# Optimization experiments

Hardware: AMD Instinct MI355X
Metric: run time of the kernel (lower is better)

## Reference

```python
import jax, jax.numpy as jnp
import numpy as np

B, C, H, W = 4, 96, 56, 56
K0, K1, DIL, HID = 5, 7, 3, 4  # HID: ConvMlp(dim, expansion, drop) => hidden_features = int(mlp_ratio) = 4 (repo quirk)
EPS = 1e-5


def _conv(x, w, b, pad, dil=1, groups=1):
    y = jax.lax.conv_general_dilated(x, w, (1, 1), [(pad, pad), (pad, pad)],
                                     rhs_dilation=(dil, dil),
                                     dimension_numbers=('NCHW', 'OIHW', 'NCHW'),
                                     feature_group_count=groups)
    return y + b[None, :, None, None]


def _conv1x1(x, w, b):
    return jnp.einsum('bchw,oc->bohw', x, w) + b[None, :, None, None]


def _ln(x, g, b):
    # LayerNormProxy: LayerNorm over channel dim of NCHW
    mu = jnp.mean(x, axis=1, keepdims=True)
    v = jnp.var(x, axis=1, keepdims=True)
    return (x - mu) * jax.lax.rsqrt(v + EPS) * g[None, :, None, None] + b[None, :, None, None]


def _gelu(x):
    return jax.nn.gelu(x, approximate=False)  # torch nn.GELU default = exact erf


def _deform_dw(x, ow, ob, dw, db, k, dil, pad):
    # DeformConv2d wrapper: offsets from a same-geometry conv, then depthwise deformable conv.
    Bx, Cx, Hx, Wx = x.shape
    P = k * k
    off = _conv(x, ow, ob, pad, dil).reshape(Bx, P, 2, Hx, Wx)  # [B,P,(y,x),H,W]
    ky = (jnp.repeat(jnp.arange(k), k) * dil - pad).astype(x.dtype)  # row-major kernel grid
    kx = (jnp.tile(jnp.arange(k), k) * dil - pad).astype(x.dtype)
    py = jnp.arange(Hx, dtype=x.dtype)[None, None, :, None] + ky[None, :, None, None] + off[:, :, 0]
    px = jnp.arange(Wx, dtype=x.dtype)[None, None, None, :] + kx[None, :, None, None] + off[:, :, 1]
    y0 = jnp.floor(py)
    x0 = jnp.floor(px)
    wy = py - y0
    wx = px - x0
    xf = x.reshape(Bx, Cx, Hx * Wx)

    def corner(yi, xi):
        valid = (yi >= 0) & (yi < Hx) & (xi >= 0) & (xi < Wx)
        idx = (jnp.clip(yi, 0, Hx - 1).astype(jnp.int32) * Wx
               + jnp.clip(xi, 0, Wx - 1).astype(jnp.int32)).reshape(Bx, -1)
        g = jax.vmap(lambda a, i: jnp.take(a, i, axis=1))(xf, idx).reshape(Bx, Cx, P, Hx, Wx)
        return g * valid[:, None].astype(x.dtype)

    v = (corner(y0, x0) * ((1 - wy) * (1 - wx))[:, None]
         + corner(y0, x0 + 1) * ((1 - wy) * wx)[:, None]
         + corner(y0 + 1, x0) * (wy * (1 - wx))[:, None]
         + corner(y0 + 1, x0 + 1) * (wy * wx)[:, None])  # [B,C,P,H,W]
    return jnp.einsum('bcphw,cp->bchw', v, dw) + db[None, :, None, None]


def setup_inputs() -> dict:
    key = jax.random.key(0)
    ks = iter(jax.random.split(key, 32))

    def rn(shape, s=1.0):
        return jax.random.normal(next(ks), shape, jnp.float32) * s

    f32 = jnp.float32
    return {
        'x': rn((B, C, H, W)),
        'g1n': jnp.ones((C,), f32), 'b1n': jnp.zeros((C,), f32),
        'p1w': rn((C, C), 1 / np.sqrt(C)), 'p1b': jnp.zeros((C,), f32),
        'o0w': rn((2 * K0 * K0, C, K0, K0), 0.05 / np.sqrt(C * K0 * K0)), 'o0b': jnp.zeros((2 * K0 * K0,), f32),
        'd0w': rn((C, K0 * K0), 1 / np.sqrt(K0 * K0)), 'd0b': jnp.zeros((C,), f32),
        'o1w': rn((2 * K1 * K1, C, K1, K1), 0.05 / np.sqrt(C * K1 * K1)), 'o1b': jnp.zeros((2 * K1 * K1,), f32),
        'd1w': rn((C, K1 * K1), 1 / np.sqrt(K1 * K1)), 'd1b': jnp.zeros((C,), f32),
        'c1w': rn((C, C), 1 / np.sqrt(C)), 'c1b': jnp.zeros((C,), f32),
        'p2w': rn((C, C), 1 / np.sqrt(C)), 'p2b': jnp.zeros((C,), f32),
        'ls1': jnp.full((C,), 0.01, f32),
        'g2n': jnp.ones((C,), f32), 'b2n': jnp.zeros((C,), f32),
        'f1w': rn((HID, C), 1 / np.sqrt(C)), 'f1b': jnp.zeros((HID,), f32),
        'dww': rn((HID, 1, 3, 3), 1 / 3.0), 'dwb': jnp.zeros((HID,), f32),
        'f2w': rn((C, HID), 1 / np.sqrt(HID)), 'f2b': jnp.zeros((C,), f32),
        'ls2': jnp.full((C,), 0.01, f32),
    }


def reference(x, g1n, b1n, p1w, p1b, o0w, o0b, d0w, d0b, o1w, o1b, d1w, d1b,
              c1w, c1b, p2w, p2b, ls1, g2n, b2n, f1w, f1b, dww, dwb, f2w, f2b, ls2):
    # attention branch
    y = _ln(x, g1n, b1n)
    shortcut = y
    y = _gelu(_conv1x1(y, p1w, p1b))
    u = y
    a = _deform_dw(y, o0w, o0b, d0w, d0b, K0, 1, K0 // 2)
    a = _deform_dw(a, o1w, o1b, d1w, d1b, K1, DIL, (K1 // 2) * DIL)
    a = _conv1x1(a, c1w, c1b)
    y = _conv1x1(u * a, p2w, p2b) + shortcut
    y = ls1[None, :, None, None] * y
    x = x + y
    # MLP branch (note: norm2 is applied to the branch output y, as in the source)
    z = _ln(y, g2n, b2n)
    z = _conv1x1(z, f1w, f1b)
    z = _gelu(_conv(z, dww, dwb, 1, 1, HID))
    z = _conv1x1(z, f2w, f2b)
    x = x + ls2[None, :, None, None] * z
    return x
```

## Files before the change

kernel.cpp:

```cpp
#include <hip/hip_runtime.h>
#include <math.h>

namespace {

constexpr int Bc = 4, Cc = 96, Hc = 56, Wc = 56;
constexpr int HWc = Hc * Wc;
constexpr int Nc  = Bc * HWc;
constexpr float EPSc = 1e-5f;

typedef __attribute__((ext_vector_type(8))) short bf16x8;
typedef __attribute__((ext_vector_type(4))) float f32x4;

__device__ __forceinline__ unsigned short f2bf(float f) {
  union { float f; unsigned u; } x; x.f = f;
  unsigned r = x.u + 0x7fffu + ((x.u >> 16) & 1u);
  return (unsigned short)(r >> 16);
}
__device__ __forceinline__ float bf2f(unsigned short u) {
  union { unsigned u; float f; } x; x.u = (unsigned)u << 16; return x.f;
}
__device__ __forceinline__ float gelu_exact(float x) {
  return 0.5f * x * (1.0f + erff(x * 0.7071067811865475f));
}

__global__ __launch_bounds__(256) void k_ln(const float* __restrict__ x,
                                            const float* __restrict__ g,
                                            const float* __restrict__ b,
                                            unsigned short* __restrict__ outN) {
  int pos = blockIdx.x * 256 + threadIdx.x;
  int bb = pos / HWc, hw = pos % HWc;
  const float* xb = x + (size_t)bb * Cc * HWc + hw;
  float s = 0.f, s2 = 0.f;
  for (int c = 0; c < Cc; ++c) { float v = xb[c * HWc]; s += v; s2 += v * v; }
  float mu  = s * (1.f / Cc);
  float var = fmaxf(s2 * (1.f / Cc) - mu * mu, 0.f);
  float rs  = rsqrtf(var + EPSc);
  unsigned short* ob = outN + (size_t)pos * Cc;
  for (int q = 0; q < 12; ++q) {
    unsigned short t8[8];
#pragma unroll
    for (int j = 0; j < 8; ++j) {
      int c = q * 8 + j;
      t8[j] = f2bf((xb[c * HWc] - mu) * rs * g[c] + b[c]);
    }
    *reinterpret_cast<bf16x8*>(ob + q * 8) = *reinterpret_cast<const bf16x8*>(t8);
  }
}

template <int K_, int MTILES, int P>
__global__ __launch_bounds__(256) void k_pack_w(const float* __restrict__ wsrc,
                                                unsigned short* __restrict__ wpk) {
  constexpr int TOTAL = K_ * K_ * 3 * MTILES * 512;
  int idx = blockIdx.x * 256 + threadIdx.x;
  if (idx >= TOTAL) return;
  int j    = idx & 7;
  int lane = (idx >> 3) & 63;
  int t    = idx >> 9;
  int mt   = t % MTILES;
  int step = t / MTILES;
  int o = mt * 16 + (lane & 15);
  int k = step * 32 + ((lane >> 4) & 3) * 8 + j;
  int p = k / Cc, c = k % Cc;
  float v = 0.f;
  if (o < P) v = wsrc[(((size_t)o * Cc + c) * K_ + p / K_) * K_ + (p % K_)];
  wpk[idx] = f2bf(v);
}

__global__ __launch_bounds__(256) void k_pack_dwt(const float* __restrict__ dwsrc,
                                                  float* __restrict__ dwt, int KK) {
  int idx = blockIdx.x * 256 + threadIdx.x;
  if (idx >= KK * Cc) return;
  int p = idx / Cc, c = idx % Cc;
  dwt[idx] = dwsrc[c * KK + p];
}

template <int GELU, int PADP, int WP>
__global__ __launch_bounds__(256) void k_pwg(const unsigned short* __restrict__ inN,
                                             const unsigned short* __restrict__ wpk,
                                             const float* __restrict__ bq,
                                             unsigned short* __restrict__ outPad) {
  int lane = threadIdx.x & 63;
  int wv = threadIdx.x >> 6;
  int ng = wv & 1, mg = wv >> 1;
  int n = blockIdx.x * 32 + ng * 16 + (lane & 15);
  int ko = ((lane >> 4) & 3) * 8;
  const unsigned short* ib = inN + (size_t)n * Cc + ko;
  const unsigned short* wl = wpk + (size_t)lane * 8;
  f32x4 acc[3];
#pragma unroll
  for (int m = 0; m < 3; ++m) acc[m] = (f32x4){0.f, 0.f, 0.f, 0.f};
#pragma unroll
  for (int ks = 0; ks < 3; ++ks) {
    bf16x8 bf = *reinterpret_cast<const bf16x8*>(ib + ks * 32);
#pragma unroll
    for (int m = 0; m < 3; ++m) {
      bf16x8 af = *reinterpret_cast<const bf16x8*>(wl + (size_t)(ks * 6 + mg * 3 + m) * 512);
      acc[m] = __builtin_amdgcn_mfma_f32_16x16x32_bf16(af, bf, acc[m], 0, 0, 0);
    }
  }
  int bb = n / HWc, hw = n % HWc;
  int h = hw / Wc, w = hw % Wc;
  unsigned short* ob = outPad + (((size_t)bb * (Hc + 2 * PADP) + h + PADP) * WP + w + PADP) * Cc;
  int orow = ((lane >> 4) & 3) * 4;
#pragma unroll
  for (int m = 0; m < 3; ++m) {
    int o0 = (mg * 3 + m) * 16 + orow;
    float4 bv = *reinterpret_cast<const float4*>(bq + o0);
    unsigned short t4[4];
#pragma unroll
    for (int j = 0; j < 4; ++j) {
      float r = acc[m][j] + ((const float*)&bv)[j];
      if (GELU) r = gelu_exact(r);
      t4[j] = f2bf(r);
    }
    *reinterpret_cast<uint2*>(ob + o0) = *reinterpret_cast<const uint2*>(t4);
  }
}

template <int UPADP, int UWP>
__global__ __launch_bounds__(256) void k_comb(const unsigned short* __restrict__ uPad,
                                              const unsigned short* __restrict__ An,
                                              const unsigned short* __restrict__ wpk,
                                              const float* __restrict__ bq,
                                              const unsigned short* __restrict__ ylnN,
                                              const float* __restrict__ ls1q,
                                              const float* __restrict__ x,
                                              float* __restrict__ out,
                                              unsigned short* __restrict__ y2N) {
  int lane = threadIdx.x & 63;
  int wv = threadIdx.x >> 6;
  int ng = wv & 1, mg = wv >> 1;
  int n = blockIdx.x * 32 + ng * 16 + (lane & 15);
  int ko = ((lane >> 4) & 3) * 8;
  int bb = n / HWc, hw = n % HWc;
  int h = hw / Wc, w = hw % Wc;
  const unsigned short* ub = uPad + (((size_t)bb * (Hc + 2 * UPADP) + h + UPADP) * UWP + w + UPADP) * Cc + ko;
  const unsigned short* ab = An + (size_t)n * Cc + ko;
  const unsigned short* wl = wpk + (size_t)lane * 8;
  f32x4 acc[3];
#pragma unroll
  for (int m = 0; m < 3; ++m) acc[m] = (f32x4){0.f, 0.f, 0.f, 0.f};
#pragma unroll
  for (int ks = 0; ks < 3; ++ks) {
    bf16x8 uv = *reinterpret_cast<const bf16x8*>(ub + ks * 32);
    bf16x8 av = *reinterpret_cast<const bf16x8*>(ab + ks * 32);
    union { bf16x8 v; unsigned short s[8]; } uu, aa, gg;
    uu.v = uv; aa.v = av;
#pragma unroll
    for (int j = 0; j < 8; ++j) gg.s[j] = f2bf(bf2f(uu.s[j]) * bf2f(aa.s[j]));
#pragma unroll
    for (int m = 0; m < 3; ++m) {
      bf16x8 af = *reinterpret_cast<const bf16x8*>(wl + (size_t)(ks * 6 + mg * 3 + m) * 512);
      acc[m] = __builtin_amdgcn_mfma_f32_16x16x32_bf16(af, gg.v, acc[m], 0, 0, 0);
    }
  }
  int orow = ((lane >> 4) & 3) * 4;
  const float* xb = x + (size_t)bb * Cc * HWc + hw;
  float* ob = out + (size_t)bb * Cc * HWc + hw;
#pragma unroll
  for (int m = 0; m < 3; ++m) {
    int o0 = (mg * 3 + m) * 16 + orow;
    float4 bv = *reinterpret_cast<const float4*>(bq + o0);
    float4 lv = *reinterpret_cast<const float4*>(ls1q + o0);
    uint2 yl = *reinterpret_cast<const uint2*>(ylnN + (size_t)n * Cc + o0);
    unsigned short yl4[4];
    *reinterpret_cast<uint2*>(yl4) = yl;
    unsigned short t4[4];
#pragma unroll
    for (int j = 0; j < 4; ++j) {
      float t = acc[m][j] + ((const float*)&bv)[j] + bf2f(yl4[j]);
      float y2 = ((const float*)&lv)[j] * t;
      t4[j] = f2bf(y2);
      ob[(size_t)(o0 + j) * HWc] = xb[(size_t)(o0 + j) * HWc] + y2;
    }
    *reinterpret_cast<uint2*>(y2N + (size_t)n * Cc + o0) = *reinterpret_cast<const uint2*>(t4);
  }
}

template <int K_, int DIL_, int MTILES, int MT, int P, int PADP, int WP, int PSTR, int SPLIT>
__global__ __launch_bounds__(256) void k_conv_mfma(const unsigned short* __restrict__ inp,
                                                   const unsigned short* __restrict__ wpk,
                                                   const float* __restrict__ bq,
                                                   float* __restrict__ dstT) {
  constexpr int KK = K_ * K_;
  constexpr int KKbase = KK / SPLIT, KKrem = KK % SPLIT;
  constexpr int HP = Hc + 2 * PADP;
  constexpr int NBLK = Nc / 32;
  int lane = threadIdx.x & 63;
  int wv = threadIdx.x >> 6;
  int bid = blockIdx.x;
  int sp = blockIdx.y;
  int p0 = sp * KKbase + min(sp, KKrem);
  int pcnt = KKbase + (sp < KKrem ? 1 : 0);
  int ntile = (bid & 7) * (NBLK / 8) + (bid >> 3);
  int n0 = ntile * 32 + (lane & 15);
  int n1 = n0 + 16;
  int b0 = n0 / HWc, hw0 = n0 % HWc, h0 = hw0 / Wc, w0 = hw0 % Wc;
  int b1 = n1 / HWc, hw1 = n1 % HWc, h1 = hw1 / Wc, w1 = hw1 % Wc;
  int co = ((lane >> 4) & 3) * 8;
  const unsigned short* ib0 = inp + ((size_t)b0 * HP * WP + (size_t)h0 * WP + w0) * Cc + co;
  const unsigned short* ib1 = inp + ((size_t)b1 * HP * WP + (size_t)h1 * WP + w1) * Cc + co;
  const unsigned short* wl = wpk + (size_t)lane * 8;
  int mt0 = wv * MT;
  int mtc[MT];
#pragma unroll
  for (int i = 0; i < MT; ++i) mtc[i] = min(mt0 + i, MTILES - 1);

  f32x4 acc[MT][2];
#pragma unroll
  for (int i = 0; i < MT; ++i) {
    acc[i][0] = (f32x4){0.f, 0.f, 0.f, 0.f};
    acc[i][1] = (f32x4){0.f, 0.f, 0.f, 0.f};
  }

  bf16x8 Bb[3][2], Aa[MT][3];
  {
    size_t toff = (size_t)((p0 / K_) * DIL_ * WP + (p0 % K_) * DIL_) * Cc;
#pragma unroll
    for (int cc = 0; cc < 3; ++cc) {
      Bb[cc][0] = *reinterpret_cast<const bf16x8*>(ib0 + toff + cc * 32);
      Bb[cc][1] = *reinterpret_cast<const bf16x8*>(ib1 + toff + cc * 32);
#pragma unroll
      for (int i = 0; i < MT; ++i)
        Aa[i][cc] = *reinterpret_cast<const bf16x8*>(wl + ((size_t)(p0 * 3 + cc) * MTILES + mtc[i]) * 512);
    }
  }

#pragma unroll 2
  for (int pi = 0; pi < pcnt; ++pi) {
    int pn = p0 + ((pi + 1 < pcnt) ? pi + 1 : pi);
    size_t toff = (size_t)((pn / K_) * DIL_ * WP + (pn % K_) * DIL_) * Cc;
    const unsigned short* sp0 = ib0 + toff;
    const unsigned short* sp1 = ib1 + toff;
    bf16x8 Bn[3][2], An[MT][3];
#pragma unroll
    for (int cc = 0; cc < 3; ++cc) {
      Bn[cc][0] = *reinterpret_cast<const bf16x8*>(sp0 + cc * 32);
      Bn[cc][1] = *reinterpret_cast<const bf16x8*>(sp1 + cc * 32);
#pragma unroll
      for (int i = 0; i < MT; ++i)
        An[i][cc] = *reinterpret_cast<const bf16x8*>(wl + ((size_t)(pn * 3 + cc) * MTILES + mtc[i]) * 512);
    }
#pragma unroll
    for (int cc = 0; cc < 3; ++cc)
#pragma unroll
      for (int i = 0; i < MT; ++i) {
        acc[i][0] = __builtin_amdgcn_mfma_f32_16x16x32_bf16(Aa[i][cc], Bb[cc][0], acc[i][0], 0, 0, 0);
        acc[i][1] = __builtin_amdgcn_mfma_f32_16x16x32_bf16(Aa[i][cc], Bb[cc][1], acc[i][1], 0, 0, 0);
      }
#pragma unroll
    for (int cc = 0; cc < 3; ++cc) {
      Bb[cc][0] = Bn[cc][0];
      Bb[cc][1] = Bn[cc][1];
#pragma unroll
      for (int i = 0; i < MT; ++i) Aa[i][cc] = An[i][cc];
    }
  }

  float* dsp = dstT + (size_t)sp * Nc * PSTR;
  int orow = ((lane >> 4) & 3) * 4;
#pragma unroll
  for (int i = 0; i < MT; ++i) {
    int mt = mt0 + i;
    if (mt >= MTILES) break;
#pragma unroll
    for (int nt = 0; nt < 2; ++nt) {
      float4 st;
#pragma unroll
      for (int j = 0; j < 4; ++j) {
        int o = mt * 16 + orow + j;
        float bias = (sp == 0 && o < P) ? bq[o] : 0.f;
        ((float*)&st)[j] = acc[i][nt][j] + bias;
      }
      int n = nt ? n1 : n0;
      *reinterpret_cast<float4*>(dsp + (size_t)n * PSTR + mt * 16 + orow) = st;
    }
  }
}

template <int K_, int DIL_, int PAD_, int IPADP, int IWP, int OPADP, int OWP, int PSTR, int NSUM>
__global__ __launch_bounds__(256) void k_deform(const unsigned short* __restrict__ srcT,
                                                const float* __restrict__ offT,
                                                const float* __restrict__ dwt,
                                                const float* __restrict__ dbq,
                                                float* __restrict__ dst,
                                                unsigned short* __restrict__ dstPad) {
  constexpr int KK = K_ * K_;
  constexpr int KK4 = KK & ~3;
  constexpr int IHP = Hc + 2 * IPADP;
  int tid = blockIdx.x * 256 + threadIdx.x;
  int cg = tid % 24;
  int pos = tid / 24;
  int c = cg * 4;
  int bb = pos / HWc, hw = pos % HWc;
  int h = hw / Wc, w = hw % Wc;
  const unsigned short* sb = srcT + (size_t)bb * IHP * IWP * Cc + c;
  const float* ob = offT + (size_t)pos * PSTR;
  float ax = 0.f, ay = 0.f, az = 0.f, aw = 0.f;

  for (int pg = 0; pg < KK4; pg += 4) {
    float4 o01 = *reinterpret_cast<const float4*>(ob + 2 * pg);
    float4 o23 = *reinterpret_cast<const float4*>(ob + 2 * pg + 4);
#pragma unroll
    for (int q = 1; q < NSUM; ++q) {
      const float* obq = ob + (size_t)q * Nc * PSTR;
      float4 a01 = *reinterpret_cast<const float4*>(obq + 2 * pg);
      float4 a23 = *reinterpret_cast<const float4*>(obq + 2 * pg + 4);
      o01.x += a01.x; o01.y += a01.y; o01.z += a01.z; o01.w += a01.w;
      o23.x += a23.x; o23.y += a23.y; o23.z += a23.z; o23.w += a23.w;
    }
    float oyv[4] = {o01.x, o01.z, o23.x, o23.z};
    float oxv[4] = {o01.y, o01.w, o23.y, o23.w};
    uint2 v[4][4];
    float wt[4][4];
#pragma unroll
    for (int i = 0; i < 4; ++i) {
      int p = pg + i;
      float py = (float)(h + (p / K_) * DIL_ - PAD_) + oyv[i];
      float px = (float)(w + (p % K_) * DIL_ - PAD_) + oxv[i];
      float y0f = floorf(py), x0f = floorf(px);
      float wy = py - y0f, wx = px - x0f;
      int y0 = (int)y0f, x0 = (int)x0f;
#pragma unroll
      for (int dy = 0; dy < 2; ++dy) {
        int yi = y0 + dy;
        bool yv = (unsigned)yi < (unsigned)Hc;
        int yc = min(max(yi, 0), Hc - 1);
        float wyv = dy ? wy : 1.f - wy;
#pragma unroll
        for (int dx = 0; dx < 2; ++dx) {
          int xi = x0 + dx;
          bool xv = (unsigned)xi < (unsigned)Wc;
          int xc = min(max(xi, 0), Wc - 1);
          wt[i][dy * 2 + dx] = (yv && xv) ? wyv * (dx ? wx : 1.f - wx) : 0.f;
          v[i][dy * 2 + dx] = *reinterpret_cast<const uint2*>(
              sb + ((size_t)(yc + IPADP) * IWP + (xc + IPADP)) * Cc);
        }
      }
    }
#pragma unroll
    for (int i = 0; i < 4; ++i) {
      int p = pg + i;
      float4 d = *reinterpret_cast<const float4*>(dwt + (size_t)p * Cc + c);
      float sx = 0.f, sy = 0.f, sz = 0.f, sw = 0.f;
#pragma unroll
      for (int q = 0; q < 4; ++q) {
        float wq_ = wt[i][q];
        sx += wq_ * bf2f((unsigned short)(v[i][q].x & 0xffffu));
        sy += wq_ * bf2f((unsigned short)(v[i][q].x >> 16));
        sz += wq_ * bf2f((unsigned short)(v[i][q].y & 0xffffu));
        sw += wq_ * bf2f((unsigned short)(v[i][q].y >> 16));
      }
      ax += sx * d.x; ay += sy * d.y; az += sz * d.z; aw += sw * d.w;
    }
  }
  {
    int p = KK - 1;
    float oy = ob[2 * p], ox = ob[2 * p + 1];
#pragma unroll
    for (int q = 1; q < NSUM; ++q) {
      const float* obq = ob + (size_t)q * Nc * PSTR;
      oy += obq[2 * p]; ox += obq[2 * p + 1];
    }
    float py = (float)(h + (p / K_) * DIL_ - PAD_) + oy;
    float px = (float)(w + (p % K_) * DIL_ - PAD_) + ox;
    float y0f = floorf(py), x0f = floorf(px);
    float wy = py - y0f, wx = px - x0f;
    int y0 = (int)y0f, x0 = (int)x0f;
    uint2 v[4]; float wt[4];
#pragma unroll
    for (int dy = 0; dy < 2; ++dy) {
      int yi = y0 + dy;
      bool yv = (unsigned)yi < (unsigned)Hc;
      int yc = min(max(yi, 0), Hc - 1);
      float wyv = dy ? wy : 1.f - wy;
#pragma unroll
      for (int dx = 0; dx < 2; ++dx) {
        int xi = x0 + dx;
        bool xv = (unsigned)xi < (unsigned)Wc;
        int xc = min(max(xi, 0), Wc - 1);
        wt[dy * 2 + dx] = (yv && xv) ? wyv * (dx ? wx : 1.f - wx) : 0.f;
        v[dy * 2 + dx] = *reinterpret_cast<const uint2*>(
            sb + ((size_t)(yc + IPADP) * IWP + (xc + IPADP)) * Cc);
      }
    }
    float4 d = *reinterpret_cast<const float4*>(dwt + (size_t)p * Cc + c);
    float sx = 0.f, sy = 0.f, sz = 0.f, sw = 0.f;
#pragma unroll
    for (int q = 0; q < 4; ++q) {
      sx += wt[q] * bf2f((unsigned short)(v[q].x & 0xffffu));
      sy += wt[q] * bf2f((unsigned short)(v[q].x >> 16));
      sz += wt[q] * bf2f((unsigned short)(v[q].y & 0xffffu));
      sw += wt[q] * bf2f((unsigned short)(v[q].y >> 16));
    }
    ax += sx * d.x; ay += sy * d.y; az += sz * d.z; aw += sw * d.w;
  }

  ax += dbq[c]; ay += dbq[c + 1]; az += dbq[c + 2]; aw += dbq[c + 3];
  if (dst) {
    float* d = dst + (size_t)bb * Cc * HWc + hw;
    d[(c + 0) * HWc] = ax; d[(c + 1) * HWc] = ay;
    d[(c + 2) * HWc] = az; d[(c + 3) * HWc] = aw;
  }
  if (dstPad) {
    unsigned short t4[4] = {f2bf(ax), f2bf(ay), f2bf(az), f2bf(aw)};
    unsigned short* tb = dstPad + (((size_t)bb * (Hc + 2 * OPADP) + h + OPADP) * OWP + w + OPADP) * Cc + c;
    *reinterpret_cast<uint2*>(tb) = *reinterpret_cast<const uint2*>(t4);
  }
}

__global__ __launch_bounds__(256) void k_mlp1(const unsigned short* __restrict__ y2N,
                                              const float* __restrict__ g,
                                              const float* __restrict__ b,
                                              const float* __restrict__ f1wq,
                                              const float* __restrict__ f1bq,
                                              float* __restrict__ z4) {
  int pos = blockIdx.x * 256 + threadIdx.x;
  int bb = pos / HWc, hw = pos % HWc;
  const unsigned short* yb = y2N + (size_t)pos * Cc;
  float vv[96];
  float s = 0.f, s2 = 0.f;
#pragma unroll
  for (int q = 0; q < 12; ++q) {
    bf16x8 t = *reinterpret_cast<const bf16x8*>(yb + q * 8);
    union { bf16x8 v; unsigned short s[8]; } u; u.v = t;
#pragma unroll
    for (int j = 0; j < 8; ++j) {
      float f = bf2f(u.s[j]);
      vv[q * 8 + j] = f; s += f; s2 += f * f;
    }
  }
  float mu  = s * (1.f / Cc);
  float var = fmaxf(s2 * (1.f / Cc) - mu * mu, 0.f);
  float rs  = rsqrtf(var + EPSc);
  float a0 = 0.f, a1 = 0.f, a2 = 0.f, a3 = 0.f;
#pragma unroll
  for (int c = 0; c < 96; ++c) {
    float t = (vv[c] - mu) * rs * g[c] + b[c];
    a0 += t * f1wq[0 * Cc + c];
    a1 += t * f1wq[1 * Cc + c];
    a2 += t * f1wq[2 * Cc + c];
    a3 += t * f1wq[3 * Cc + c];
  }
  float* zb = z4 + (size_t)bb * 4 * HWc + hw;
  zb[0 * HWc] = a0 + f1bq[0];
  zb[1 * HWc] = a1 + f1bq[1];
  zb[2 * HWc] = a2 + f1bq[2];
  zb[3 * HWc] = a3 + f1bq[3];
}

__global__ __launch_bounds__(256) void k_mlp_dw(const float* __restrict__ z4,
                                                const float* __restrict__ dwwq,
                                                const float* __restrict__ dwbq,
                                                float* __restrict__ z4b) {
  int tid = blockIdx.x * 256 + threadIdx.x;
  int hw = tid % HWc;
  int bj = tid / HWc;
  int j = bj % 4;
  int h = hw / Wc, w = hw % Wc;
  const float* zb = z4 + (size_t)bj * HWc;
  float s = 0.f;
#pragma unroll
  for (int ky = 0; ky < 3; ++ky) {
    int y = h + ky - 1;
    if ((unsigned)y >= (unsigned)Hc) continue;
#pragma unroll
    for (int kx = 0; kx < 3; ++kx) {
      int x = w + kx - 1;
      if ((unsigned)x >= (unsigned)Wc) continue;
      s += zb[y * Wc + x] * dwwq[j * 9 + ky * 3 + kx];
    }
  }
  z4b[tid] = gelu_exact(s + dwbq[j]);
}

__global__ __launch_bounds__(256) void k_mlp2(const float* __restrict__ z4b,
                                              const float* __restrict__ f2wq,
                                              const float* __restrict__ f2bq,
                                              const float* __restrict__ ls2q,
                                              float* __restrict__ out) {
  int pos = blockIdx.x * 256 + threadIdx.x;
  int bb = pos / HWc, hw = pos % HWc;
  const float* zb = z4b + (size_t)bb * 4 * HWc + hw;
  float z0 = zb[0 * HWc], z1 = zb[1 * HWc], z2 = zb[2 * HWc], z3 = zb[3 * HWc];
  float* ob = out + (size_t)bb * Cc * HWc + hw;
  for (int o = 0; o < Cc; ++o) {
    float s = f2bq[o] + z0 * f2wq[o * 4 + 0] + z1 * f2wq[o * 4 + 1]
                      + z2 * f2wq[o * 4 + 2] + z3 * f2wq[o * 4 + 3];
    ob[o * HWc] += ls2q[o] * s;
  }
}

}

extern "C" void kernel_launch(void* const* d_in, const int* in_sizes, int n_in,
                              void* d_out, int out_size, void* d_ws, size_t ws_size,
                              hipStream_t stream) {
  (void)in_sizes; (void)n_in; (void)out_size; (void)ws_size;
  const float* x   = (const float*)d_in[0];
  const float* g1n = (const float*)d_in[1];
  const float* b1n = (const float*)d_in[2];
  const float* p1w = (const float*)d_in[3];
  const float* p1b = (const float*)d_in[4];
  const float* o0w = (const float*)d_in[5];
  const float* o0b = (const float*)d_in[6];
  const float* d0w = (const float*)d_in[7];
  const float* d0b = (const float*)d_in[8];
  const float* o1w = (const float*)d_in[9];
  const float* o1b = (const float*)d_in[10];
  const float* d1w = (const float*)d_in[11];
  const float* d1b = (const float*)d_in[12];
  const float* c1w = (const float*)d_in[13];
  const float* c1b = (const float*)d_in[14];
  const float* p2w = (const float*)d_in[15];
  const float* p2b = (const float*)d_in[16];
  const float* ls1 = (const float*)d_in[17];
  const float* g2n = (const float*)d_in[18];
  const float* b2n = (const float*)d_in[19];
  const float* f1w = (const float*)d_in[20];
  const float* f1b = (const float*)d_in[21];
  const float* dww = (const float*)d_in[22];
  const float* dwb = (const float*)d_in[23];
  const float* f2w = (const float*)d_in[24];
  const float* f2b = (const float*)d_in[25];
  const float* ls2 = (const float*)d_in[26];
  float* out = (float*)d_out;
  float* ws  = (float*)d_ws;

  float* off0t = ws;                                  size_t o_ = (size_t)2 * Nc * 64;
  float* off1t = ws + o_;                             o_ += (size_t)4 * Nc * 112;
  float* z4    = ws + o_;                             o_ += (size_t)Bc * 4 * HWc;
  float* z4b   = ws + o_;                             o_ += (size_t)Bc * 4 * HWc;
  float* dwt0  = ws + o_;                             o_ += 25 * Cc;
  float* dwt1  = ws + o_;                             o_ += 49 * Cc;
  unsigned short* yln_n  = (unsigned short*)(ws + o_); o_ += (size_t)Nc * Cc / 2;
  unsigned short* a1_n   = (unsigned short*)(ws + o_); o_ += (size_t)Nc * Cc / 2;
  unsigned short* A_n    = (unsigned short*)(ws + o_); o_ += (size_t)Nc * Cc / 2;
  unsigned short* y2_n   = (unsigned short*)(ws + o_); o_ += (size_t)Nc * Cc / 2;
  unsigned short* u_pad  = (unsigned short*)(ws + o_); o_ += (size_t)Bc * 60 * 60 * Cc / 2;
  unsigned short* a0_pad = (unsigned short*)(ws + o_); o_ += (size_t)Bc * 74 * 74 * Cc / 2;
  unsigned short* wpk0   = (unsigned short*)(ws + o_); o_ += (size_t)25 * 3 * 4 * 512 / 2;
  unsigned short* wpk1   = (unsigned short*)(ws + o_); o_ += (size_t)49 * 3 * 7 * 512 / 2;
  unsigned short* wpkp1  = (unsigned short*)(ws + o_); o_ += (size_t)3 * 6 * 512 / 2;
  unsigned short* wpkc1  = (unsigned short*)(ws + o_); o_ += (size_t)3 * 6 * 512 / 2;
  unsigned short* wpkp2  = (unsigned short*)(ws + o_); o_ += (size_t)3 * 6 * 512 / 2;

  dim3 b256(256, 1, 1);

  hipMemsetAsync(u_pad, 0, (size_t)Bc * 60 * 60 * Cc * sizeof(unsigned short), stream);
  hipMemsetAsync(a0_pad, 0, (size_t)Bc * 74 * 74 * Cc * sizeof(unsigned short), stream);
  hipLaunchKernelGGL((k_pack_w<5, 4, 50>), dim3((25 * 3 * 4 * 512 + 255) / 256), b256, 0, stream, o0w, wpk0);
  hipLaunchKernelGGL((k_pack_w<7, 7, 98>), dim3((49 * 3 * 7 * 512 + 255) / 256), b256, 0, stream, o1w, wpk1);
  hipLaunchKernelGGL((k_pack_w<1, 6, 96>), dim3((3 * 6 * 512 + 255) / 256), b256, 0, stream, p1w, wpkp1);
  hipLaunchKernelGGL((k_pack_w<1, 6, 96>), dim3((3 * 6 * 512 + 255) / 256), b256, 0, stream, c1w, wpkc1);
  hipLaunchKernelGGL((k_pack_w<1, 6, 96>), dim3((3 * 6 * 512 + 255) / 256), b256, 0, stream, p2w, wpkp2);
  hipLaunchKernelGGL(k_pack_dwt, dim3((25 * Cc + 255) / 256), b256, 0, stream, d0w, dwt0, 25);
  hipLaunchKernelGGL(k_pack_dwt, dim3((49 * Cc + 255) / 256), b256, 0, stream, d1w, dwt1, 49);

  hipLaunchKernelGGL(k_ln, dim3(Nc / 256), b256, 0, stream, x, g1n, b1n, yln_n);
  hipLaunchKernelGGL((k_pwg<1, 2, 60>), dim3(Nc / 32), b256, 0, stream, yln_n, wpkp1, p1b, u_pad);
  hipLaunchKernelGGL((k_conv_mfma<5, 1, 4, 1, 50, 2, 60, 64, 2>), dim3(Nc / 32, 2), b256, 0, stream,
                     u_pad, wpk0, o0b, off0t);
  hipLaunchKernelGGL((k_deform<5, 1, 2, 2, 60, 9, 74, 64, 2>), dim3(Nc * 24 / 256), b256, 0, stream,
                     u_pad, off0t, dwt0, d0b, (float*)nullptr, a0_pad);
  hipLaunchKernelGGL((k_conv_mfma<7, 3, 7, 2, 98, 9, 74, 112, 4>), dim3(Nc / 32, 4), b256, 0, stream,
                     a0_pad, wpk1, o1b, off1t);
  hipLaunchKernelGGL((k_deform<7, 3, 9, 9, 74, 0, 56, 112, 4>), dim3(Nc * 24 / 256), b256, 0, stream,
                     a0_pad, off1t, dwt1, d1b, (float*)nullptr, a1_n);
  hipLaunchKernelGGL((k_pwg<0, 0, 56>), dim3(Nc / 32), b256, 0, stream, a1_n, wpkc1, c1b, A_n);
  hipLaunchKernelGGL((k_comb<2, 60>), dim3(Nc / 32), b256, 0, stream,
                     u_pad, A_n, wpkp2, p2b, yln_n, ls1, x, out, y2_n);
  hipLaunchKernelGGL(k_mlp1, dim3(Nc / 256), b256, 0, stream, y2_n, g2n, b2n, f1w, f1b, z4);
  hipLaunchKernelGGL(k_mlp_dw, dim3(Nc * 4 / 256), b256, 0, stream, z4, dww, dwb, z4b);
  hipLaunchKernelGGL(k_mlp2, dim3(Nc / 256), b256, 0, stream, z4b, f2w, f2b, ls2, out);
}
```

Before: 233.8 us.

## Split deformable conv into metadata precompute pass and wider-channel gather kernel

Adds a k_meta kernel that computes, once per (position, tap), the summed offsets, clamped corner indices and validity-masked bilinear weights. These are written to workspace buffers. The deform kernel then reads this metadata and gathers 8 bf16 channels per thread with 16-byte loads instead of 4 channels with 8-byte loads. This removes the offset reduction and coordinate math that was repeated across all 24 channel groups. The cost is an extra launch and a round trip of metadata through global memory, about 24 bytes per tap per position.

```diff
diff --git a/kernel.cpp b/kernel.cpp
--- a/kernel.cpp
+++ b/kernel.cpp
@@ -278,135 +278,108 @@
   }
 }
 
-template <int K_, int DIL_, int PAD_, int IPADP, int IWP, int OPADP, int OWP, int PSTR, int NSUM>
-__global__ __launch_bounds__(256) void k_deform(const unsigned short* __restrict__ srcT,
-                                                const float* __restrict__ offT,
-                                                const float* __restrict__ dwt,
-                                                const float* __restrict__ dbq,
-                                                float* __restrict__ dst,
-                                                unsigned short* __restrict__ dstPad) {
+template <int K_, int DIL_, int PAD_, int PSTR, int NSUM>
+__global__ __launch_bounds__(256) void k_meta(const float* __restrict__ offT,
+                                              uint2* __restrict__ metaI,
+                                              float4* __restrict__ metaW) {
   constexpr int KK = K_ * K_;
-  constexpr int KK4 = KK & ~3;
+  int idx = blockIdx.x * 256 + threadIdx.x;
+  if (idx >= Nc * KK) return;
+  int p = idx % KK, pos = idx / KK;
+  int hw = pos % HWc;
+  int h = hw / Wc, w = hw % Wc;
+  const float* ob = offT + (size_t)pos * PSTR + 2 * p;
+  float oy = ob[0], ox = ob[1];
+#pragma unroll
+  for (int q = 1; q < NSUM; ++q) {
+    oy += ob[(size_t)q * Nc * PSTR];
+    ox += ob[(size_t)q * Nc * PSTR + 1];
+  }
+  float py = (float)(h + (p / K_) * DIL_ - PAD_) + oy;
+  float px = (float)(w + (p % K_) * DIL_ - PAD_) + ox;
+  float y0f = floorf(py), x0f = floorf(px);
+  float wy = py - y0f, wx = px - x0f;
+  int y0 = (int)y0f, x0 = (int)x0f;
+  int y1 = y0 + 1, x1 = x0 + 1;
+  bool y0v = (unsigned)y0 < (unsigned)Hc, y1v = (unsigned)y1 < (unsigned)Hc;
+  bool x0v = (unsigned)x0 < (unsigned)Wc, x1v = (unsigned)x1 < (unsigned)Wc;
+  int y0c = min(max(y0, 0), Hc - 1), y1c = min(max(y1, 0), Hc - 1);
+  int x0c = min(max(x0, 0), Wc - 1), x1c = min(max(x1, 0), Wc - 1);
+  uint2 mi;
+  mi.x = (unsigned)(y0c | (y1c << 16));
+  mi.y = (unsigned)(x0c | (x1c << 16));
+  float4 mw;
+  mw.x = (y0v && x0v) ? (1.f - wy) * (1.f - wx) : 0.f;
+  mw.y = (y0v && x1v) ? (1.f - wy) * wx : 0.f;
+  mw.z = (y1v && x0v) ? wy * (1.f - wx) : 0.f;
+  mw.w = (y1v && x1v) ? wy * wx : 0.f;
+  metaI[idx] = mi;
+  metaW[idx] = mw;
+}
+
+template <int K_, int IPADP, int IWP, int OPADP, int OWP>
+__global__ __launch_bounds__(256) void k_deform2(const unsigned short* __restrict__ srcT,
+                                                 const uint2* __restrict__ metaI,
+                                                 const float4* __restrict__ metaW,
+                                                 const float* __restrict__ dwt,
+                                                 const float* __restrict__ dbq,
+                                                 unsigned short* __restrict__ dstPad) {
+  constexpr int KK = K_ * K_;
   constexpr int IHP = Hc + 2 * IPADP;
   int tid = blockIdx.x * 256 + threadIdx.x;
-  int cg = tid % 24;
-  int pos = tid / 24;
-  int c = cg * 4;
+  int cg = tid % 12;
+  int pos = tid / 12;
+  int c = cg * 8;
   int bb = pos / HWc, hw = pos % HWc;
   int h = hw / Wc, w = hw % Wc;
   const unsigned short* sb = srcT + (size_t)bb * IHP * IWP * Cc + c;
-  const float* ob = offT + (size_t)pos * PSTR;
-  float ax = 0.f, ay = 0.f, az = 0.f, aw = 0.f;
-
-  for (int pg = 0; pg < KK4; pg += 4) {
-    float4 o01 = *reinterpret_cast<const float4*>(ob + 2 * pg);
-    float4 o23 = *reinterpret_cast<const float4*>(ob + 2 * pg + 4);
-#pragma unroll
-    for (int q = 1; q < NSUM; ++q) {
-      const float* obq = ob + (size_t)q * Nc * PSTR;
-      float4 a01 = *reinterpret_cast<const float4*>(obq + 2 * pg);
-      float4 a23 = *reinterpret_cast<const float4*>(obq + 2 * pg + 4);
-      o01.x += a01.x; o01.y += a01.y; o01.z += a01.z; o01.w += a01.w;
-      o23.x += a23.x; o23.y += a23.y; o23.z += a23.z; o23.w += a23.w;
-    }
-    float oyv[4] = {o01.x, o01.z, o23.x, o23.z};
-    float oxv[4] = {o01.y, o01.w, o23.y, o23.w};
-    uint2 v[4][4];
-    float wt[4][4];
-#pragma unroll
-    for (int i = 0; i < 4; ++i) {
-      int p = pg + i;
-      float py = (float)(h + (p / K_) * DIL_ - PAD_) + oyv[i];
-      float px = (float)(w + (p % K_) * DIL_ - PAD_) + oxv[i];
-      float y0f = floorf(py), x0f = floorf(px);
-      float wy = py - y0f, wx = px - x0f;
-      int y0 = (int)y0f, x0 = (int)x0f;
-#pragma unroll
-      for (int dy = 0; dy < 2; ++dy) {
-        int yi = y0 + dy;
-        bool yv = (unsigned)yi < (unsigned)Hc;
-        int yc = min(max(yi, 0), Hc - 1);
-        float wyv = dy ? wy : 1.f - wy;
-#pragma unroll
-        for (int dx = 0; dx < 2; ++dx) {
-          int xi = x0 + dx;
-          bool xv = (unsigned)xi < (unsigned)Wc;
-          int xc = min(max(xi, 0), Wc - 1);
-          wt[i][dy * 2 + dx] = (yv && xv) ? wyv * (dx ? wx : 1.f - wx) : 0.f;
-          v[i][dy * 2 + dx] = *reinterpret_cast<const uint2*>(
-              sb + ((size_t)(yc + IPADP) * IWP + (xc + IPADP)) * Cc);
-        }
-      }
-    }
-#pragma unroll
-    for (int i = 0; i < 4; ++i) {
-      int p = pg + i;
-      float4 d = *reinterpret_cast<const float4*>(dwt + (size_t)p * Cc + c);
-      float sx = 0.f, sy = 0.f, sz = 0.f, sw = 0.f;
-#pragma unroll
-      for (int q = 0; q < 4; ++q) {
-        float wq_ = wt[i][q];
-        sx += wq_ * bf2f((unsigned short)(v[i][q].x & 0xffffu));
-        sy += wq_ * bf2f((unsigned short)(v[i][q].x >> 16));
-        sz += wq_ * bf2f((unsigned short)(v[i][q].y & 0xffffu));
-        sw += wq_ * bf2f((unsigned short)(v[i][q].y >> 16));
-      }
-      ax += sx * d.x; ay += sy * d.y; az += sz * d.z; aw += sw * d.w;
-    }
-  }
-  {
-    int p = KK - 1;
-    float oy = ob[2 * p], ox = ob[2 * p + 1];
-#pragma unroll
-    for (int q = 1; q < NSUM; ++q) {
-      const float* obq = ob + (size_t)q * Nc * PSTR;
-      oy += obq[2 * p]; ox += obq[2 * p + 1];
-    }
-    float py = (float)(h + (p / K_) * DIL_ - PAD_) + oy;
-    float px = (float)(w + (p % K_) * DIL_ - PAD_) + ox;
-    float y0f = floorf(py), x0f = floorf(px);
-    float wy = py - y0f, wx = px - x0f;
-    int y0 = (int)y0f, x0 = (int)x0f;
-    uint2 v[4]; float wt[4];
-#pragma unroll
-    for (int dy = 0; dy < 2; ++dy) {
-      int yi = y0 + dy;
-      bool yv = (unsigned)yi < (unsigned)Hc;
-      int yc = min(max(yi, 0), Hc - 1);
-      float wyv = dy ? wy : 1.f - wy;
-#pragma unroll
-      for (int dx = 0; dx < 2; ++dx) {
-        int xi = x0 + dx;
-        bool xv = (unsigned)xi < (unsigned)Wc;
-        int xc = min(max(xi, 0), Wc - 1);
-        wt[dy * 2 + dx] = (yv && xv) ? wyv * (dx ? wx : 1.f - wx) : 0.f;
-        v[dy * 2 + dx] = *reinterpret_cast<const uint2*>(
-            sb + ((size_t)(yc + IPADP) * IWP + (xc + IPADP)) * Cc);
-      }
-    }
-    float4 d = *reinterpret_cast<const float4*>(dwt + (size_t)p * Cc + c);
-    float sx = 0.f, sy = 0.f, sz = 0.f, sw = 0.f;
-#pragma unroll
-    for (int q = 0; q < 4; ++q) {
-      sx += wt[q] * bf2f((unsigned short)(v[q].x & 0xffffu));
-      sy += wt[q] * bf2f((unsigned short)(v[q].x >> 16));
-      sz += wt[q] * bf2f((unsigned short)(v[q].y & 0xffffu));
-      sw += wt[q] * bf2f((unsigned short)(v[q].y >> 16));
-    }
-    ax += sx * d.x; ay += sy * d.y; az += sz * d.z; aw += sw * d.w;
-  }
-
-  ax += dbq[c]; ay += dbq[c + 1]; az += dbq[c + 2]; aw += dbq[c + 3];
-  if (dst) {
-    float* d = dst + (size_t)bb * Cc * HWc + hw;
-    d[(c + 0) * HWc] = ax; d[(c + 1) * HWc] = ay;
-    d[(c + 2) * HWc] = az; d[(c + 3) * HWc] = aw;
-  }
-  if (dstPad) {
-    unsigned short t4[4] = {f2bf(ax), f2bf(ay), f2bf(az), f2bf(aw)};
-    unsigned short* tb = dstPad + (((size_t)bb * (Hc + 2 * OPADP) + h + OPADP) * OWP + w + OPADP) * Cc + c;
-    *reinterpret_cast<uint2*>(tb) = *reinterpret_cast<const uint2*>(t4);
-  }
+  const uint2* mi = metaI + (size_t)pos * KK;
+  const float4* mw = metaW + (size_t)pos * KK;
+  float acc[8];
+#pragma unroll
+  for (int j = 0; j < 8; ++j) acc[j] = 0.f;
+
+  auto tap = [&](int p, uint2 I, float4 W) {
+    int y0 = (int)(I.x & 0xffffu) + IPADP, y1 = (int)(I.x >> 16) + IPADP;
+    int x0 = (int)(I.y & 0xffffu) + IPADP, x1 = (int)(I.y >> 16) + IPADP;
+    int r0 = y0 * IWP, r1 = y1 * IWP;
+    const uint4 v00 = *reinterpret_cast<const uint4*>(sb + (size_t)(r0 + x0) * Cc);
+    const uint4 v01 = *reinterpret_cast<const uint4*>(sb + (size_t)(r0 + x1) * Cc);
+    const uint4 v10 = *reinterpret_cast<const uint4*>(sb + (size_t)(r1 + x0) * Cc);
+    const uint4 v11 = *reinterpret_cast<const uint4*>(sb + (size_t)(r1 + x1) * Cc);
+    float4 d0 = *reinterpret_cast<const float4*>(dwt + (size_t)p * Cc + c);
+    float4 d1 = *reinterpret_cast<const float4*>(dwt + (size_t)p * Cc + c + 4);
+    float dv[8] = {d0.x, d0.y, d0.z, d0.w, d1.x, d1.y, d1.z, d1.w};
+#pragma unroll
+    for (int j = 0; j < 4; ++j) {
+      unsigned u00 = ((const unsigned*)&v00)[j], u01 = ((const unsigned*)&v01)[j];
+      unsigned u10 = ((const unsigned*)&v10)[j], u11 = ((const unsigned*)&v11)[j];
+      union { unsigned u; float f; } a0_, b0_, a1_, b1_, a2_, b2_, a3_, b3_;
+      a0_.u = u00 << 16; b0_.u = u00 & 0xffff0000u;
+      a1_.u = u01 << 16; b1_.u = u01 & 0xffff0000u;
+      a2_.u = u10 << 16; b2_.u = u10 & 0xffff0000u;
+      a3_.u = u11 << 16; b3_.u = u11 & 0xffff0000u;
+      float lo = W.x * a0_.f + W.y * a1_.f + W.z * a2_.f + W.w * a3_.f;
+      float hi = W.x * b0_.f + W.y * b1_.f + W.z * b2_.f + W.w * b3_.f;
+      acc[2 * j]     += lo * dv[2 * j];
+      acc[2 * j + 1] += hi * dv[2 * j + 1];
+    }
+  };
+
+  int p = 0;
+  for (; p + 1 < KK; p += 2) {
+    uint2 I0 = mi[p], I1 = mi[p + 1];
+    float4 W0 = mw[p], W1 = mw[p + 1];
+    tap(p, I0, W0);
+    tap(p + 1, I1, W1);
+  }
+  { uint2 I = mi[p]; float4 W = mw[p]; tap(p, I, W); }
+
+  unsigned short t8[8];
+#pragma unroll
+  for (int j = 0; j < 8; ++j) t8[j] = f2bf(acc[j] + dbq[c + j]);
+  unsigned short* tb = dstPad + (((size_t)bb * (Hc + 2 * OPADP) + h + OPADP) * OWP + w + OPADP) * Cc + c;
+  *reinterpret_cast<bf16x8*>(tb) = *reinterpret_cast<const bf16x8*>(t8);
 }
 
 __global__ __launch_bounds__(256) void k_mlp1(const unsigned short* __restrict__ y2N,
@@ -532,7 +505,12 @@
   float* z4    = ws + o_;                             o_ += (size_t)Bc * 4 * HWc;
   float* z4b   = ws + o_;                             o_ += (size_t)Bc * 4 * HWc;
   float* dwt0  = ws + o_;                             o_ += 25 * Cc;
-  float* dwt1  = ws + o_;                             o_ += 49 * Cc;
+  float* dwt1  = ws + o_;                             o_ += 49 * Cc + 4;
+  o_ &= ~(size_t)3;
+  uint2*  metaI0 = (uint2*)(ws + o_);                 o_ += (size_t)Nc * 25 * 2;
+  float4* metaW0 = (float4*)(ws + o_);                o_ += (size_t)Nc * 25 * 4;
+  uint2*  metaI1 = (uint2*)(ws + o_);                 o_ += (size_t)Nc * 49 * 2;
+  float4* metaW1 = (float4*)(ws + o_);                o_ += (size_t)Nc * 49 * 4;
   unsigned short* yln_n  = (unsigned short*)(ws + o_); o_ += (size_t)Nc * Cc / 2;
   unsigned short* a1_n   = (unsigned short*)(ws + o_); o_ += (size_t)Nc * Cc / 2;
   unsigned short* A_n    = (unsigned short*)(ws + o_); o_ += (size_t)Nc * Cc / 2;
@@ -561,12 +539,16 @@
   hipLaunchKernelGGL((k_pwg<1, 2, 60>), dim3(Nc / 32), b256, 0, stream, yln_n, wpkp1, p1b, u_pad);
   hipLaunchKernelGGL((k_conv_mfma<5, 1, 4, 1, 50, 2, 60, 64, 2>), dim3(Nc / 32, 2), b256, 0, stream,
                      u_pad, wpk0, o0b, off0t);
-  hipLaunchKernelGGL((k_deform<5, 1, 2, 2, 60, 9, 74, 64, 2>), dim3(Nc * 24 / 256), b256, 0, stream,
-                     u_pad, off0t, dwt0, d0b, (float*)nullptr, a0_pad);
+  hipLaunchKernelGGL((k_meta<5, 1, 2, 64, 2>), dim3((Nc * 25 + 255) / 256), b256, 0, stream,
+                     off0t, metaI0, metaW0);
+  hipLaunchKernelGGL((k_deform2<5, 2, 60, 9, 74>), dim3(Nc * 12 / 256), b256, 0, stream,
+                     u_pad, metaI0, metaW0, dwt0, d0b, a0_pad);
   hipLaunchKernelGGL((k_conv_mfma<7, 3, 7, 2, 98, 9, 74, 112, 4>), dim3(Nc / 32, 4), b256, 0, stream,
                      a0_pad, wpk1, o1b, off1t);
-  hipLaunchKernelGGL((k_deform<7, 3, 9, 9, 74, 0, 56, 112, 4>), dim3(Nc * 24 / 256), b256, 0, stream,
-                     a0_pad, off1t, dwt1, d1b, (float*)nullptr, a1_n);
+  hipLaunchKernelGGL((k_meta<7, 3, 9, 112, 4>), dim3((Nc * 49 + 255) / 256), b256, 0, stream,
+                     off1t, metaI1, metaW1);
+  hipLaunchKernelGGL((k_deform2<7, 9, 74, 0, 56>), dim3(Nc * 12 / 256), b256, 0, stream,
+                     a0_pad, metaI1, metaW1, dwt1, d1b, a1_n);
   hipLaunchKernelGGL((k_pwg<0, 0, 56>), dim3(Nc / 32), b256, 0, stream, a1_n, wpkc1, c1b, A_n);
   hipLaunchKernelGGL((k_comb<2, 60>), dim3(Nc / 32), b256, 0, stream,
                      u_pad, A_n, wpkp2, p2b, yln_n, ls1, x, out, y2_n);
```

Measured after the change: 255.2 us. 1.09x slower.
